# Kernel tuning notes

Hardware: AMD Instinct MI355X
Metric: run time of the kernel (lower is better)

## Reference

```python
import jax, jax.numpy as jnp
import numpy as np

N_NODES = 50000
N_EDGES = 200000
EMB = 256
N_LAYERS = 2
PRED_IN = 2 * EMB + 2 * N_LAYERS * EMB  # 1536


def _glorot(key, shape):
    fan_in, fan_out = shape
    lim = (6.0 / (fan_in + fan_out)) ** 0.5
    return jax.random.uniform(key, shape, jnp.float32, -lim, lim)


def setup_inputs() -> dict:
    key = jax.random.key(0)
    ks = jax.random.split(key, 16)
    inp = {
        "entity_embd": jax.random.normal(ks[0], (N_NODES, EMB), jnp.float32),
        "edge_attr": jax.random.normal(ks[1], (N_EDGES, EMB), jnp.float32),
        "q_embd": jax.random.normal(ks[2], (1, EMB), jnp.float32),
        "noise": jax.random.uniform(ks[3], (N_EDGES, 1), jnp.float32, 1e-10, 1.0 - 1e-10),
        # proj_reverse: Linear(emb,emb) -> ReLU -> Linear(emb,emb)
        "W_pr1": _glorot(ks[4], (EMB, EMB)), "b_pr1": jnp.zeros((EMB,), jnp.float32),
        "W_pr2": _glorot(ks[5], (EMB, EMB)), "b_pr2": jnp.zeros((EMB,), jnp.float32),
        # SAGE layers: Linear(concat[self, agg]) per layer
        "sage_W0": _glorot(ks[6], (2 * EMB, EMB)), "sage_b0": jnp.zeros((EMB,), jnp.float32),
        "sage_W1": _glorot(ks[7], (2 * EMB, EMB)), "sage_b1": jnp.zeros((EMB,), jnp.float32),
        # pred: Linear(pred_in, emb) -> ReLU -> Linear(emb, 1)
        "pred_W1": _glorot(ks[8], (PRED_IN, EMB)), "pred_b1": jnp.zeros((EMB,), jnp.float32),
        "pred_W2": _glorot(ks[9], (EMB, 1)), "pred_b2": jnp.zeros((1,), jnp.float32),
        "edge_index": jax.random.randint(ks[10], (2, N_EDGES), 0, N_NODES, jnp.int64),
    }
    return inp


def _segment_mean(msg, dst, num_nodes):
    s = jax.ops.segment_sum(msg, dst, num_segments=num_nodes)
    cnt = jax.ops.segment_sum(jnp.ones((dst.shape[0], 1), msg.dtype), dst, num_segments=num_nodes)
    return s / jnp.maximum(cnt, 1.0)


def reference(entity_embd, edge_attr, q_embd, noise,
              W_pr1, b_pr1, W_pr2, b_pr2,
              sage_W0, sage_b0, sage_W1, sage_b1,
              pred_W1, pred_b1, pred_W2, pred_b2,
              edge_index):
    h_id, t_id = edge_index[0], edge_index[1]
    # bidirectional edge list: original + reversed
    ei = jnp.concatenate([edge_index, edge_index[::-1]], axis=1)  # [2, 2E]
    src, dst = ei[0], ei[1]
    # reverse-edge feature projection
    ea_rev = jax.nn.relu(edge_attr @ W_pr1 + b_pr1) @ W_pr2 + b_pr2
    h_r = jnp.concatenate([edge_attr, ea_rev], axis=0)  # [2E, EMB]
    # SAGE backbone: mean-aggregate (src + edge feat), concat with self, linear+relu
    x = entity_embd
    outs = []
    for W, b in ((sage_W0, sage_b0), (sage_W1, sage_b1)):
        msg = x[src] + h_r                                # [2E, EMB]
        agg = _segment_mean(msg, dst, N_NODES)            # [N, EMB]
        x = jax.nn.relu(jnp.concatenate([x, agg], axis=1) @ W + b)
        outs.append(x)
    h_e = jnp.concatenate(outs, axis=1)  # [N, N_LAYERS*EMB]
    q = jnp.broadcast_to(q_embd, (N_EDGES, EMB))
    h_triple = jnp.concatenate([q, h_e[h_id], edge_attr, h_e[t_id]], axis=1)  # [E, 1536]
    logits = jax.nn.relu(h_triple @ pred_W1 + pred_b1) @ pred_W2 + pred_b2    # [E, 1]
    # idp-bern sampling (training=True, temp=1)
    rn = jnp.log(noise) - jnp.log(1.0 - noise)
    sampled = jax.nn.sigmoid(logits + rn)
    return (logits, sampled)
```

## Files before the change

### kernel.cpp

```cpp
#include <hip/hip_runtime.h>
#include <math.h>


namespace {
constexpr int E    = 200000;
constexpr int NV   = 50000;
constexpr int D    = 256;
constexpr int TWOE = 2 * E;
}

typedef __attribute__((ext_vector_type(8))) _Float16 f16x8;
typedef __attribute__((ext_vector_type(4))) _Float16 f16x4;
typedef __attribute__((ext_vector_type(16))) float f32x16;

#define MFMA16(a, b, c) __builtin_amdgcn_mfma_f32_32x32x16_f16((a), (b), (c), 0, 0, 0)

typedef const __attribute__((address_space(1))) void* gas_t;
typedef __attribute__((address_space(3))) void* las_t;

__device__ inline void gload16(const void* g, void* l) {
  __builtin_amdgcn_global_load_lds((gas_t)g, (las_t)l, 16, 0, 0);
}

__global__ void k_detect(const void* ei_raw, int* flag) {
  __shared__ int bad;
  if (threadIdx.x == 0) bad = 0;
  __syncthreads();
  const long long* p = (const long long*)ei_raw;
  long long v = p[threadIdx.x];
  if (v < 0 || v >= (long long)NV) atomicOr(&bad, 1);
  __syncthreads();
  if (threadIdx.x == 0) *flag = bad ? 0 : 1;
}

__global__ void k_convert(const void* ei_raw, const int* __restrict__ flag,
                          int* __restrict__ ei32) {
  int i = blockIdx.x * 256 + threadIdx.x;
  if (i >= TWOE) return;
  if (*flag) ei32[i] = (int)((const long long*)ei_raw)[i];
  else       ei32[i] = ((const int*)ei_raw)[i];
}

__global__ void k_deg(const int* __restrict__ ei32, int* __restrict__ deg) {
  int de = blockIdx.x * 256 + threadIdx.x;
  if (de >= TWOE) return;
  int dst = (de < E) ? ei32[E + de] : ei32[de - E];
  atomicAdd(&deg[dst], 1);
}

__global__ __launch_bounds__(1024) void k_scan(const int* __restrict__ deg,
                                               int* __restrict__ off) {
  __shared__ int wsum[16];
  __shared__ int carryS;
  int tid = threadIdx.x;
  int lane = tid & 63, wv = tid >> 6;
  if (tid == 0) carryS = 0;
  __syncthreads();
  for (int base = 0; base < NV; base += 1024) {
    int i = base + tid;
    int v = (i < NV) ? deg[i] : 0;
    int s = v;
#pragma unroll
    for (int d = 1; d < 64; d <<= 1) {
      int t = __shfl_up(s, d);
      if (lane >= d) s += t;
    }
    if (lane == 63) wsum[wv] = s;
    int carry = carryS;
    __syncthreads();
    if (wv == 0) {
      int ws = (lane < 16) ? wsum[lane] : 0;
#pragma unroll
      for (int d = 1; d < 16; d <<= 1) {
        int t = __shfl_up(ws, d);
        if (lane >= d) ws += t;
      }
      if (lane < 16) wsum[lane] = ws;
    }
    __syncthreads();
    int wexcl = (wv == 0) ? 0 : wsum[wv - 1];
    if (i < NV) off[i] = carry + wexcl + s - v;
    if (tid == 1023) carryS = carry + wsum[15];
    __syncthreads();
  }
  if (tid == 0) off[NV] = carryS;
}

__global__ void k_fill(const int* __restrict__ ei32, const int* __restrict__ off,
                       int* __restrict__ cursor, int* __restrict__ eidA,
                       int* __restrict__ srcA) {
  int de = blockIdx.x * 256 + threadIdx.x;
  if (de >= TWOE) return;
  int dst = (de < E) ? ei32[E + de] : ei32[de - E];
  int p = atomicAdd(&cursor[dst], 1);
  int idx = off[dst] + p;
  eidA[idx] = de;
  srcA[idx] = ei32[de];
}

__global__ void k_rinv(const int* __restrict__ off, float* __restrict__ rinv) {
  int n = blockIdx.x * 256 + threadIdx.x;
  if (n < NV) {
    int d = off[n + 1] - off[n];
    rinv[n] = 1.f / fmaxf((float)d, 1.f);
  }
}

__global__ void k_conv16(const float* __restrict__ x, _Float16* __restrict__ y,
                         int n8) {
  int i = blockIdx.x * 256 + threadIdx.x;
  if (i >= n8) return;
  const float4* p = (const float4*)x;
  float4 a = p[2 * i], b = p[2 * i + 1];
  f16x8 o;
  o[0] = (_Float16)a.x; o[1] = (_Float16)a.y; o[2] = (_Float16)a.z; o[3] = (_Float16)a.w;
  o[4] = (_Float16)b.x; o[5] = (_Float16)b.y; o[6] = (_Float16)b.z; o[7] = (_Float16)b.w;
  ((f16x8*)y)[i] = o;
}

__global__ __launch_bounds__(256) void k_gath_h(
    const _Float16* __restrict__ ea16, const _Float16* __restrict__ tmp16,
    const _Float16* __restrict__ ent16,
    const int* __restrict__ eidA, const int* __restrict__ srcA,
    const int* __restrict__ off,
    _Float16* __restrict__ hsum16, _Float16* __restrict__ hid16,
    _Float16* __restrict__ xsum16, float* __restrict__ degrev) {
  int n = blockIdx.x * 8 + (threadIdx.x >> 5);
  if (n >= NV) return;
  int l = threadIdx.x & 31;
  float fs[8], hv[8], xs[8];
#pragma unroll
  for (int k2 = 0; k2 < 8; k2++) { fs[k2] = 0.f; hv[k2] = 0.f; xs[k2] = 0.f; }
  int o0 = off[n], o1 = off[n + 1];
  int dr = 0;
#pragma unroll 2
  for (int j = o0; j < o1; j++) {
    int de = eidA[j];
    int src = srcA[j];
    f16x8 xv = ((const f16x8*)(ent16 + (size_t)src * D))[l];
#pragma unroll
    for (int k2 = 0; k2 < 8; k2++) xs[k2] += (float)xv[k2];
    if (de < E) {
      f16x8 v = ((const f16x8*)(ea16 + (size_t)de * D))[l];
#pragma unroll
      for (int k2 = 0; k2 < 8; k2++) fs[k2] += (float)v[k2];
    } else {
      f16x8 v = ((const f16x8*)(tmp16 + (size_t)(de - E) * D))[l];
#pragma unroll
      for (int k2 = 0; k2 < 8; k2++) hv[k2] += (float)v[k2];
      dr++;
    }
  }
  f16x8 of, oh, ox;
#pragma unroll
  for (int k2 = 0; k2 < 8; k2++) {
    of[k2] = (_Float16)fs[k2]; oh[k2] = (_Float16)hv[k2]; ox[k2] = (_Float16)xs[k2];
  }
  ((f16x8*)(hsum16 + (size_t)n * D))[l] = of;
  ((f16x8*)(hid16 + (size_t)n * D))[l] = oh;
  ((f16x8*)(xsum16 + (size_t)n * D))[l] = ox;
  if (l == 0) degrev[n] = (float)dr;
}

__global__ __launch_bounds__(256) void k_agg(
    const _Float16* __restrict__ x16, const int* __restrict__ srcA,
    const int* __restrict__ off, const _Float16* __restrict__ hsum16,
    const float* __restrict__ rinv, _Float16* __restrict__ agg16) {
  int n = blockIdx.x * 8 + (threadIdx.x >> 5);
  if (n >= NV) return;
  int l = threadIdx.x & 31;
  f16x8 h = ((const f16x8*)(hsum16 + (size_t)n * D))[l];
  float s[8];
#pragma unroll
  for (int k2 = 0; k2 < 8; k2++) s[k2] = (float)h[k2];
  int o0 = off[n], o1 = off[n + 1];
#pragma unroll 4
  for (int j = o0; j < o1; j++) {
    int src = srcA[j];
    f16x8 v = ((const f16x8*)(x16 + (size_t)src * D))[l];
#pragma unroll
    for (int k2 = 0; k2 < 8; k2++) s[k2] += (float)v[k2];
  }
  float r = rinv[n];
  f16x8 o;
#pragma unroll
  for (int k2 = 0; k2 < 8; k2++) o[k2] = (_Float16)(s[k2] * r);
  ((f16x8*)(agg16 + (size_t)n * D))[l] = o;
}

__global__ __launch_bounds__(256) void k_wprep(const float* __restrict__ W,
                                               _Float16* __restrict__ Wf) {
  __shared__ float tl[32][260];
  int tid = threadIdx.x;
  int k0 = blockIdx.x * 32;
#pragma unroll
  for (int i = 0; i < 32; i++) tl[i][tid] = W[(size_t)(k0 + i) * 256 + tid];
  __syncthreads();
  f16x8* WfV = (f16x8*)Wf;
#pragma unroll
  for (int kg = 0; kg < 4; kg++) {
    f16x8 p;
#pragma unroll
    for (int j = 0; j < 8; j++) p[j] = (_Float16)tl[kg * 8 + j][tid];
    WfV[(size_t)((k0 >> 3) + kg) * 256 + tid] = p;
  }
}

__global__ void k_qw(const float* __restrict__ q, const float* __restrict__ W1,
                     const float* __restrict__ b1, float* __restrict__ qW) {
  __shared__ float ql[D];
  int n = threadIdx.x;
  ql[n] = q[n];
  __syncthreads();
  float s = b1[n];
  for (int k = 0; k < D; k++) s += ql[k] * W1[(size_t)k * D + n];
  qW[n] = s;
}

enum AM { AF16, AF16D };
enum EP { EP_RELU16, EP_ADDC, EP_HE2, EP_PROJ2 };

template<int AMODE>
__device__ inline void stageA(const _Float16* __restrict__ A0,
                              const _Float16* __restrict__ A1,
                              int m0, int t, int tid, _Float16* ldsbuf) {
  const _Float16* src;
  int kbase;
  if (AMODE == AF16D && t >= 4) { src = A1; kbase = (t - 4) * 64; }
  else                          { src = A0; kbase = t * 64; }
  const int l  = tid & 63;
  const int w  = tid >> 6;
  const int r8 = l >> 3;
  const int kg = (l & 7) ^ r8;
#pragma unroll
  for (int j = 0; j < 2; j++) {
    const int c = w * 2 + j;
    const int row = c * 8 + r8;
    gload16(src + (size_t)(m0 + row) * 256 + kbase + kg * 8,
            ldsbuf + c * 512);
  }
}

template<int AMODE, int EPI>
__global__ __launch_bounds__(256, ((EPI == EP_HE2 || EPI == EP_PROJ2) ? 2 : 4))
void k_gemm(
    const _Float16* __restrict__ A0, const _Float16* __restrict__ A1,
    const _Float16* __restrict__ addm16, const _Float16* __restrict__ xs16,
    const float* __restrict__ degrev, const float* __restrict__ rinv,
    const _Float16* __restrict__ Wf, const _Float16* __restrict__ Wf2,
    const float* __restrict__ bias, const float* __restrict__ qW,
    _Float16* __restrict__ o16a, _Float16* __restrict__ o16b, int M, int K) {
  constexpr bool DUAL = (EPI == EP_HE2 || EPI == EP_PROJ2);
  __shared__ _Float16 AS[2 * 4096];
  const int tid = threadIdx.x;
  const int w = tid >> 6;
  const int lane31 = tid & 31;
  const int hw = (tid >> 5) & 1;
  const int m0 = blockIdx.x * 64;
  const int col0 = (w << 6) + lane31;
  const int col1 = col0 + 32;

  f32x16 acc[2][2], acc2[2][2];
#pragma unroll
  for (int a = 0; a < 2; a++)
#pragma unroll
    for (int b = 0; b < 2; b++)
#pragma unroll
      for (int i = 0; i < 16; i++) { acc[a][b][i] = 0.f; acc2[a][b][i] = 0.f; }

  const f16x8* WV  = (const f16x8*)Wf;
  const f16x8* WV2 = (const f16x8*)Wf2;
  const int nt = K >> 6;
  const int sw = lane31 & 7;

  stageA<AMODE>(A0, A1, m0, 0, tid, AS);
  __syncthreads();

  for (int t = 0; t < nt; ++t) {
    const int k0 = t * 64;
    f16x8 wb0[4], wb1[4], wc0[4], wc1[4];
#pragma unroll
    for (int ks = 0; ks < 4; ks++) {
      const int kgl = 2 * ks + hw;
      size_t wi = (size_t)((k0 >> 3) + kgl) * 256;
      wb0[ks] = WV[wi + col0];
      wb1[ks] = WV[wi + col1];
      if (DUAL) { wc0[ks] = WV2[wi + col0]; wc1[ks] = WV2[wi + col1]; }
    }
    __builtin_amdgcn_sched_barrier(0);
    if (t + 1 < nt)
      stageA<AMODE>(A0, A1, m0, t + 1, tid, AS + ((t + 1) & 1) * 4096);
    __builtin_amdgcn_sched_barrier(0);
    const f16x8* cb = (const f16x8*)(AS + (t & 1) * 4096);
#pragma unroll
    for (int ks = 0; ks < 4; ks++) {
      const int kgl = 2 * ks + hw;
      f16x8 a0 = cb[lane31 * 8 + (kgl ^ sw)];
      f16x8 a1 = cb[(lane31 + 32) * 8 + (kgl ^ sw)];
      acc[0][0] = MFMA16(a0, wb0[ks], acc[0][0]);
      acc[0][1] = MFMA16(a0, wb1[ks], acc[0][1]);
      acc[1][0] = MFMA16(a1, wb0[ks], acc[1][0]);
      acc[1][1] = MFMA16(a1, wb1[ks], acc[1][1]);
      if (DUAL) {
        acc2[0][0] = MFMA16(a0, wc0[ks], acc2[0][0]);
        acc2[0][1] = MFMA16(a0, wc1[ks], acc2[0][1]);
        acc2[1][0] = MFMA16(a1, wc0[ks], acc2[1][0]);
        acc2[1][1] = MFMA16(a1, wc1[ks], acc2[1][1]);
      }
    }
    __syncthreads();
  }

  if (EPI == EP_RELU16) {
    float b0v = bias[col0], b1v = bias[col1];
#pragma unroll
    for (int rf = 0; rf < 2; rf++)
#pragma unroll
      for (int g = 0; g < 4; g++)
#pragma unroll
        for (int qq = 0; qq < 4; qq++) {
          int row = m0 + 32 * rf + qq + 8 * g + 4 * hw;
          if (row < M) {
            o16a[(size_t)row * 256 + col0] =
                (_Float16)fmaxf(acc[rf][0][4 * g + qq] + b0v, 0.f);
            o16a[(size_t)row * 256 + col1] =
                (_Float16)fmaxf(acc[rf][1][4 * g + qq] + b1v, 0.f);
          }
        }
  }
  if (EPI == EP_ADDC) {
    float b0v = bias[col0], b1v = bias[col1];
#pragma unroll
    for (int rf = 0; rf < 2; rf++)
#pragma unroll
      for (int g = 0; g < 4; g++)
#pragma unroll
        for (int qq = 0; qq < 4; qq++) {
          int row = m0 + 32 * rf + qq + 8 * g + 4 * hw;
          if (row < M) {
            float dr = degrev[row], rv = rinv[row];
            size_t i0 = (size_t)row * 256 + col0;
            size_t i1 = (size_t)row * 256 + col1;
            float h0 = acc[rf][0][4 * g + qq] + (float)addm16[i0] + dr * b0v;
            float h1 = acc[rf][1][4 * g + qq] + (float)addm16[i1] + dr * b1v;
            o16a[i0] = (_Float16)h0;
            o16a[i1] = (_Float16)h1;
            o16b[i0] = (_Float16)((h0 + (float)xs16[i0]) * rv);
            o16b[i1] = (_Float16)((h1 + (float)xs16[i1]) * rv);
          }
        }
  }
  if (EPI == EP_HE2) {
#pragma unroll
    for (int rf = 0; rf < 2; rf++)
#pragma unroll
      for (int g = 0; g < 4; g++)
#pragma unroll
        for (int qq = 0; qq < 4; qq++) {
          int row = m0 + 32 * rf + qq + 8 * g + 4 * hw;
          if (row < M) {
            o16a[(size_t)row * 256 + col0] = (_Float16)acc[rf][0][4 * g + qq];
            o16a[(size_t)row * 256 + col1] = (_Float16)acc[rf][1][4 * g + qq];
            o16b[(size_t)row * 256 + col0] = (_Float16)acc2[rf][0][4 * g + qq];
            o16b[(size_t)row * 256 + col1] = (_Float16)acc2[rf][1][4 * g + qq];
          }
        }
  }
  if (EPI == EP_PROJ2) {
    float b0v = bias[col0], b1v = bias[col1];
    float q0 = qW[col0], q1 = qW[col1];
#pragma unroll
    for (int rf = 0; rf < 2; rf++)
#pragma unroll
      for (int g = 0; g < 4; g++)
#pragma unroll
        for (int qq = 0; qq < 4; qq++) {
          int row = m0 + 32 * rf + qq + 8 * g + 4 * hw;
          if (row < M) {
            o16a[(size_t)row * 256 + col0] =
                (_Float16)fmaxf(acc[rf][0][4 * g + qq] + b0v, 0.f);
            o16a[(size_t)row * 256 + col1] =
                (_Float16)fmaxf(acc[rf][1][4 * g + qq] + b1v, 0.f);
            o16b[(size_t)row * 256 + col0] = (_Float16)(acc2[rf][0][4 * g + qq] + q0);
            o16b[(size_t)row * 256 + col1] = (_Float16)(acc2[rf][1][4 * g + qq] + q1);
          }
        }
  }
}

__global__ __launch_bounds__(256) void k_edge(
    const _Float16* __restrict__ ea2q, const _Float16* __restrict__ HEh,
    const _Float16* __restrict__ HEt, const int* __restrict__ ei32,
    const float* __restrict__ pW2, const float* __restrict__ pb2,
    const float* __restrict__ noise, float* __restrict__ dout) {
  int e = blockIdx.x * 8 + (threadIdx.x >> 5);
  int l = threadIdx.x & 31;
  int h = ei32[e], t = ei32[E + e];
  f16x8 a  = ((const f16x8*)(ea2q + (size_t)e * 256))[l];
  f16x8 hv = ((const f16x8*)(HEh + (size_t)h * 256))[l];
  f16x8 tv = ((const f16x8*)(HEt + (size_t)t * 256))[l];
  const float4* wp = (const float4*)(pW2 + l * 8);
  float4 w0 = wp[0], w1 = wp[1];
  float wv[8] = {w0.x, w0.y, w0.z, w0.w, w1.x, w1.y, w1.z, w1.w};
  float s = 0.f;
#pragma unroll
  for (int j = 0; j < 8; j++)
    s += fmaxf((float)a[j] + (float)hv[j] + (float)tv[j], 0.f) * wv[j];
#pragma unroll
  for (int m = 1; m <= 16; m <<= 1) s += __shfl_xor(s, m);
  if (l == 0) {
    float lg = s + pb2[0];
    float nz = noise[e];
    float rn = logf(nz) - logf(1.f - nz);
    dout[e] = lg;
    dout[E + e] = 1.f / (1.f + expf(-(lg + rn)));
  }
}

extern "C" void kernel_launch(void* const* d_in, const int* in_sizes, int n_in,
                              void* d_out, int out_size, void* d_ws, size_t ws_size,
                              hipStream_t stream) {
  const float* entity = (const float*)d_in[0];
  const float* ea     = (const float*)d_in[1];
  const float* q      = (const float*)d_in[2];
  const float* noise  = (const float*)d_in[3];
  const float* W_pr1  = (const float*)d_in[4];
  const float* b_pr1  = (const float*)d_in[5];
  const float* W_pr2  = (const float*)d_in[6];
  const float* b_pr2  = (const float*)d_in[7];
  const float* sW0    = (const float*)d_in[8];
  const float* sb0    = (const float*)d_in[9];
  const float* sW1    = (const float*)d_in[10];
  const float* sb1    = (const float*)d_in[11];
  const float* pW1    = (const float*)d_in[12];
  const float* pb1    = (const float*)d_in[13];
  const float* pW2    = (const float*)d_in[14];
  const float* pb2    = (const float*)d_in[15];
  const void*  ei_raw = d_in[16];

  char* ws = (char*)d_ws;
  const size_t EDH = (size_t)E * D * 2;
  const size_t NDH = (size_t)NV * D * 2;
  const size_t PAD = 64 * 256 * 2;
  size_t off_b = 0;
  char* r0  = ws + off_b; off_b += EDH + PAD;
  char* r1a = ws + off_b; off_b += EDH + PAD;
  char* r1b = ws + off_b; off_b += EDH + PAD;
  char* r2  = ws + off_b; off_b += 2 * NDH + PAD;
  char* r3  = ws + off_b; off_b += NDH + PAD;
  char* r4  = ws + off_b; off_b += NDH + PAD;
  char* r5  = ws + off_b; off_b += NDH + PAD;
  char* r6  = ws + off_b; off_b += NDH + PAD;
  auto alloc_w = [&](int K) { _Float16* p = (_Float16*)(ws + off_b);
                              off_b += (size_t)K * 256 * 2; return p; };
  _Float16* Wpr1f = alloc_w(256);
  _Float16* Wpr2f = alloc_w(256);
  _Float16* sW0f  = alloc_w(512);
  _Float16* sW1f  = alloc_w(512);
  _Float16* Whehf = alloc_w(512);
  _Float16* Whetf = alloc_w(512);
  _Float16* Weaf  = alloc_w(256);
  float* rinv   = (float*)(ws + off_b); off_b += (size_t)NV * 4;
  float* degrev = (float*)(ws + off_b); off_b += (size_t)NV * 4;
  float* qW     = (float*)(ws + off_b); off_b += 1024;
  int*   ei32   = (int*)(ws + off_b);   off_b += (size_t)TWOE * 4;
  int*   eidA   = (int*)(ws + off_b);   off_b += (size_t)TWOE * 4;
  int*   srcA   = (int*)(ws + off_b);   off_b += (size_t)TWOE * 4;
  int*   offA   = (int*)(ws + off_b);   off_b += (size_t)(NV + 1) * 4;
  int*   deg    = (int*)(ws + off_b);   off_b += (size_t)NV * 4;
  int*   cursor = (int*)(ws + off_b);   off_b += (size_t)NV * 4;
  int*   flag   = (int*)(ws + off_b);   off_b += 64;

  _Float16* ea16   = (_Float16*)r0;
  _Float16* tmp16  = (_Float16*)r1a;
  _Float16* ea2q16 = (_Float16*)r1b;
  _Float16* hsum16 = (_Float16*)r2;
  _Float16* HEh16  = (_Float16*)r2;
  _Float16* HEt16  = (_Float16*)(r2 + NDH);
  _Float16* hid16  = (_Float16*)r3;
  _Float16* agg016 = (_Float16*)r3;
  _Float16* agg16  = (_Float16*)r3;
  _Float16* ent16  = (_Float16*)r4;
  _Float16* out116 = (_Float16*)r4;
  _Float16* out016 = (_Float16*)r5;
  _Float16* xsum16 = (_Float16*)r6;

  k_detect<<<1, 256, 0, stream>>>(ei_raw, flag);
  k_convert<<<(TWOE + 255) / 256, 256, 0, stream>>>(ei_raw, flag, ei32);
  hipMemsetAsync(deg, 0, (size_t)NV * 4, stream);
  hipMemsetAsync(cursor, 0, (size_t)NV * 4, stream);
  k_deg<<<(TWOE + 255) / 256, 256, 0, stream>>>(ei32, deg);
  k_scan<<<1, 1024, 0, stream>>>(deg, offA);
  k_fill<<<(TWOE + 255) / 256, 256, 0, stream>>>(ei32, offA, cursor, eidA, srcA);
  k_rinv<<<(NV + 255) / 256, 256, 0, stream>>>(offA, rinv);

  k_wprep<<<256 / 32, 256, 0, stream>>>(W_pr1, Wpr1f);
  k_wprep<<<256 / 32, 256, 0, stream>>>(W_pr2, Wpr2f);
  k_wprep<<<512 / 32, 256, 0, stream>>>(sW0, sW0f);
  k_wprep<<<512 / 32, 256, 0, stream>>>(sW1, sW1f);
  k_wprep<<<512 / 32, 256, 0, stream>>>(pW1 + 256 * 256, Whehf);
  k_wprep<<<512 / 32, 256, 0, stream>>>(pW1 + 1024 * 256, Whetf);
  k_wprep<<<256 / 32, 256, 0, stream>>>(pW1 + 768 * 256, Weaf);
  k_conv16<<<(NV * D / 8 + 255) / 256, 256, 0, stream>>>(entity, ent16, NV * D / 8);
  k_conv16<<<(E * D / 8 + 255) / 256, 256, 0, stream>>>(ea, ea16, E * D / 8);
  k_qw<<<1, 256, 0, stream>>>(q, pW1, pb1, qW);

  k_gemm<AF16, EP_PROJ2><<<E / 64, 256, 0, stream>>>(
      ea16, nullptr, nullptr, nullptr, nullptr, nullptr, Wpr1f, Weaf,
      b_pr1, qW, tmp16, ea2q16, E, 256);

  k_gath_h<<<(NV + 7) / 8, 256, 0, stream>>>(
      ea16, tmp16, ent16, eidA, srcA, offA, hsum16, hid16, xsum16, degrev);

  k_gemm<AF16, EP_ADDC><<<(NV + 63) / 64, 256, 0, stream>>>(
      hid16, nullptr, hsum16, xsum16, degrev, rinv, Wpr2f, nullptr,
      b_pr2, nullptr, hsum16, agg016, NV, 256);

  k_gemm<AF16D, EP_RELU16><<<(NV + 63) / 64, 256, 0, stream>>>(
      ent16, agg016, nullptr, nullptr, nullptr, nullptr, sW0f, nullptr,
      sb0, nullptr, out016, nullptr, NV, 512);
  k_agg<<<(NV + 7) / 8, 256, 0, stream>>>(out016, srcA, offA, hsum16, rinv, agg16);
  k_gemm<AF16D, EP_RELU16><<<(NV + 63) / 64, 256, 0, stream>>>(
      out016, agg16, nullptr, nullptr, nullptr, nullptr, sW1f, nullptr,
      sb1, nullptr, out116, nullptr, NV, 512);

  k_gemm<AF16D, EP_HE2><<<(NV + 63) / 64, 256, 0, stream>>>(
      out016, out116, nullptr, nullptr, nullptr, nullptr, Whehf, Whetf,
      nullptr, nullptr, HEh16, HEt16, NV, 512);

  k_edge<<<E / 8, 256, 0, stream>>>(ea2q16, HEh16, HEt16, ei32, pW2, pb2, noise,
                                    (float*)d_out);
}
```

Before: 632.7 us.

## Fuse chained node-level GEMMs into two kernels keeping intermediates in LDS

```diff
diff --git a/kernel.cpp b/kernel.cpp
--- a/kernel.cpp
+++ b/kernel.cpp
@@ -218,7 +218,6 @@
 }
 
 enum AM { AF16, AF16D };
-enum EP { EP_RELU16, EP_ADDC, EP_HE2, EP_PROJ2 };
 
 template<int AMODE>
 __device__ inline void stageA(const _Float16* __restrict__ A0,
@@ -241,16 +240,11 @@
   }
 }
 
-template<int AMODE, int EPI>
-__global__ __launch_bounds__(256, ((EPI == EP_HE2 || EPI == EP_PROJ2) ? 2 : 4))
-void k_gemm(
-    const _Float16* __restrict__ A0, const _Float16* __restrict__ A1,
-    const _Float16* __restrict__ addm16, const _Float16* __restrict__ xs16,
-    const float* __restrict__ degrev, const float* __restrict__ rinv,
+__global__ __launch_bounds__(256, 2) void k_proj2(
+    const _Float16* __restrict__ A0,
     const _Float16* __restrict__ Wf, const _Float16* __restrict__ Wf2,
     const float* __restrict__ bias, const float* __restrict__ qW,
-    _Float16* __restrict__ o16a, _Float16* __restrict__ o16b, int M, int K) {
-  constexpr bool DUAL = (EPI == EP_HE2 || EPI == EP_PROJ2);
+    _Float16* __restrict__ o16a, _Float16* __restrict__ o16b, int M) {
   __shared__ _Float16 AS[2 * 4096];
   const int tid = threadIdx.x;
   const int w = tid >> 6;
@@ -259,6 +253,7 @@
   const int m0 = blockIdx.x * 64;
   const int col0 = (w << 6) + lane31;
   const int col1 = col0 + 32;
+  const int sw = lane31 & 7;
 
   f32x16 acc[2][2], acc2[2][2];
 #pragma unroll
@@ -270,26 +265,21 @@
 
   const f16x8* WV  = (const f16x8*)Wf;
   const f16x8* WV2 = (const f16x8*)Wf2;
-  const int nt = K >> 6;
-  const int sw = lane31 & 7;
-
-  stageA<AMODE>(A0, A1, m0, 0, tid, AS);
+
+  stageA<AF16>(A0, nullptr, m0, 0, tid, AS);
   __syncthreads();
-
-  for (int t = 0; t < nt; ++t) {
+  for (int t = 0; t < 4; ++t) {
     const int k0 = t * 64;
     f16x8 wb0[4], wb1[4], wc0[4], wc1[4];
 #pragma unroll
     for (int ks = 0; ks < 4; ks++) {
       const int kgl = 2 * ks + hw;
       size_t wi = (size_t)((k0 >> 3) + kgl) * 256;
-      wb0[ks] = WV[wi + col0];
-      wb1[ks] = WV[wi + col1];
-      if (DUAL) { wc0[ks] = WV2[wi + col0]; wc1[ks] = WV2[wi + col1]; }
+      wb0[ks] = WV[wi + col0];  wb1[ks] = WV[wi + col1];
+      wc0[ks] = WV2[wi + col0]; wc1[ks] = WV2[wi + col1];
     }
     __builtin_amdgcn_sched_barrier(0);
-    if (t + 1 < nt)
-      stageA<AMODE>(A0, A1, m0, t + 1, tid, AS + ((t + 1) & 1) * 4096);
+    if (t + 1 < 4) stageA<AF16>(A0, nullptr, m0, t + 1, tid, AS + ((t + 1) & 1) * 4096);
     __builtin_amdgcn_sched_barrier(0);
     const f16x8* cb = (const f16x8*)(AS + (t & 1) * 4096);
 #pragma unroll
@@ -301,18 +291,275 @@
       acc[0][1] = MFMA16(a0, wb1[ks], acc[0][1]);
       acc[1][0] = MFMA16(a1, wb0[ks], acc[1][0]);
       acc[1][1] = MFMA16(a1, wb1[ks], acc[1][1]);
-      if (DUAL) {
+      acc2[0][0] = MFMA16(a0, wc0[ks], acc2[0][0]);
+      acc2[0][1] = MFMA16(a0, wc1[ks], acc2[0][1]);
+      acc2[1][0] = MFMA16(a1, wc0[ks], acc2[1][0]);
+      acc2[1][1] = MFMA16(a1, wc1[ks], acc2[1][1]);
+    }
+    __syncthreads();
+  }
+  float b0v = bias[col0], b1v = bias[col1];
+  float q0 = qW[col0], q1 = qW[col1];
+#pragma unroll
+  for (int rf = 0; rf < 2; rf++)
+#pragma unroll
+    for (int g = 0; g < 4; g++)
+#pragma unroll
+      for (int qq = 0; qq < 4; qq++) {
+        int row = m0 + 32 * rf + qq + 8 * g + 4 * hw;
+        if (row < M) {
+          o16a[(size_t)row * 256 + col0] =
+              (_Float16)fmaxf(acc[rf][0][4 * g + qq] + b0v, 0.f);
+          o16a[(size_t)row * 256 + col1] =
+              (_Float16)fmaxf(acc[rf][1][4 * g + qq] + b1v, 0.f);
+          o16b[(size_t)row * 256 + col0] = (_Float16)(acc2[rf][0][4 * g + qq] + q0);
+          o16b[(size_t)row * 256 + col1] = (_Float16)(acc2[rf][1][4 * g + qq] + q1);
+        }
+      }
+}
+
+__global__ __launch_bounds__(256, 2) void k_fuse0(
+    const _Float16* __restrict__ hid16, const _Float16* __restrict__ ent16,
+    _Float16* __restrict__ hsum16, const _Float16* __restrict__ xsum16,
+    const float* __restrict__ degrev, const float* __restrict__ rinv,
+    const _Float16* __restrict__ Wpr2f, const float* __restrict__ bpr2,
+    const _Float16* __restrict__ sW0f, const float* __restrict__ sb0,
+    _Float16* __restrict__ out016, int M) {
+  __shared__ _Float16 AS[2 * 4096];
+  __shared__ _Float16 AGG[4 * 4096];
+  const int tid = threadIdx.x;
+  const int w = tid >> 6;
+  const int lane31 = tid & 31;
+  const int hw = (tid >> 5) & 1;
+  const int m0 = blockIdx.x * 64;
+  const int col0 = (w << 6) + lane31;
+  const int col1 = col0 + 32;
+  const int sw = lane31 & 7;
+  const int kgA = lane31 >> 3, kjA = lane31 & 7;
+
+  f32x16 acc[2][2];
+#pragma unroll
+  for (int a = 0; a < 2; a++)
+#pragma unroll
+    for (int b = 0; b < 2; b++)
+#pragma unroll
+      for (int i = 0; i < 16; i++) acc[a][b][i] = 0.f;
+
+  {
+    const f16x8* WV = (const f16x8*)Wpr2f;
+    stageA<AF16>(hid16, nullptr, m0, 0, tid, AS);
+    __syncthreads();
+    for (int t = 0; t < 4; ++t) {
+      const int k0 = t * 64;
+      f16x8 wb0[4], wb1[4];
+#pragma unroll
+      for (int ks = 0; ks < 4; ks++) {
+        const int kgl = 2 * ks + hw;
+        size_t wi = (size_t)((k0 >> 3) + kgl) * 256;
+        wb0[ks] = WV[wi + col0]; wb1[ks] = WV[wi + col1];
+      }
+      __builtin_amdgcn_sched_barrier(0);
+      if (t + 1 < 4) stageA<AF16>(hid16, nullptr, m0, t + 1, tid, AS + ((t + 1) & 1) * 4096);
+      __builtin_amdgcn_sched_barrier(0);
+      const f16x8* cb = (const f16x8*)(AS + (t & 1) * 4096);
+#pragma unroll
+      for (int ks = 0; ks < 4; ks++) {
+        const int kgl = 2 * ks + hw;
+        f16x8 a0 = cb[lane31 * 8 + (kgl ^ sw)];
+        f16x8 a1 = cb[(lane31 + 32) * 8 + (kgl ^ sw)];
+        acc[0][0] = MFMA16(a0, wb0[ks], acc[0][0]);
+        acc[0][1] = MFMA16(a0, wb1[ks], acc[0][1]);
+        acc[1][0] = MFMA16(a1, wb0[ks], acc[1][0]);
+        acc[1][1] = MFMA16(a1, wb1[ks], acc[1][1]);
+      }
+      __syncthreads();
+    }
+  }
+  stageA<AF16>(ent16, nullptr, m0, 0, tid, AS);
+  {
+    float b0v = bpr2[col0], b1v = bpr2[col1];
+    _Float16* AGGw = AGG + (w << 12);
+#pragma unroll
+    for (int rf = 0; rf < 2; rf++)
+#pragma unroll
+      for (int g = 0; g < 4; g++)
+#pragma unroll
+        for (int qq = 0; qq < 4; qq++) {
+          int rowloc = 32 * rf + qq + 8 * g + 4 * hw;
+          int row = m0 + rowloc;
+          float a0 = 0.f, a1 = 0.f;
+          if (row < M) {
+            float dr = degrev[row], rv = rinv[row];
+            size_t i0 = (size_t)row * 256 + col0;
+            size_t i1 = (size_t)row * 256 + col1;
+            float h0 = acc[rf][0][4 * g + qq] + (float)hsum16[i0] + dr * b0v;
+            float h1 = acc[rf][1][4 * g + qq] + (float)hsum16[i1] + dr * b1v;
+            hsum16[i0] = (_Float16)h0;
+            hsum16[i1] = (_Float16)h1;
+            a0 = (h0 + (float)xsum16[i0]) * rv;
+            a1 = (h1 + (float)xsum16[i1]) * rv;
+          }
+          int rsw = rowloc & 7;
+          AGGw[rowloc * 64 + ((kgA ^ rsw) << 3) + kjA] = (_Float16)a0;
+          AGGw[rowloc * 64 + (((kgA + 4) ^ rsw) << 3) + kjA] = (_Float16)a1;
+          acc[rf][0][4 * g + qq] = 0.f;
+          acc[rf][1][4 * g + qq] = 0.f;
+        }
+  }
+  __syncthreads();
+  {
+    const f16x8* WV = (const f16x8*)sW0f;
+    for (int tt = 0; tt < 8; ++tt) {
+      f16x8 wb0[4], wb1[4];
+#pragma unroll
+      for (int ks = 0; ks < 4; ks++) {
+        const int kgl = 2 * ks + hw;
+        size_t wi = (size_t)(tt * 8 + kgl) * 256;
+        wb0[ks] = WV[wi + col0]; wb1[ks] = WV[wi + col1];
+      }
+      __builtin_amdgcn_sched_barrier(0);
+      if (tt + 1 < 4) stageA<AF16>(ent16, nullptr, m0, tt + 1, tid, AS + ((tt + 1) & 1) * 4096);
+      __builtin_amdgcn_sched_barrier(0);
+      const f16x8* cb = (tt < 4) ? (const f16x8*)(AS + (tt & 1) * 4096)
+                                 : (const f16x8*)(AGG + ((tt - 4) << 12));
+#pragma unroll
+      for (int ks = 0; ks < 4; ks++) {
+        const int kgl = 2 * ks + hw;
+        f16x8 a0 = cb[lane31 * 8 + (kgl ^ sw)];
+        f16x8 a1 = cb[(lane31 + 32) * 8 + (kgl ^ sw)];
+        acc[0][0] = MFMA16(a0, wb0[ks], acc[0][0]);
+        acc[0][1] = MFMA16(a0, wb1[ks], acc[0][1]);
+        acc[1][0] = MFMA16(a1, wb0[ks], acc[1][0]);
+        acc[1][1] = MFMA16(a1, wb1[ks], acc[1][1]);
+      }
+      __syncthreads();
+    }
+    float b0v = sb0[col0], b1v = sb0[col1];
+#pragma unroll
+    for (int rf = 0; rf < 2; rf++)
+#pragma unroll
+      for (int g = 0; g < 4; g++)
+#pragma unroll
+        for (int qq = 0; qq < 4; qq++) {
+          int row = m0 + 32 * rf + qq + 8 * g + 4 * hw;
+          if (row < M) {
+            out016[(size_t)row * 256 + col0] =
+                (_Float16)fmaxf(acc[rf][0][4 * g + qq] + b0v, 0.f);
+            out016[(size_t)row * 256 + col1] =
+                (_Float16)fmaxf(acc[rf][1][4 * g + qq] + b1v, 0.f);
+          }
+        }
+  }
+}
+
+__global__ __launch_bounds__(256, 2) void k_fuse1(
+    const _Float16* __restrict__ out016, const _Float16* __restrict__ agg16,
+    const _Float16* __restrict__ sW1f, const float* __restrict__ sb1,
+    const _Float16* __restrict__ Whehf, const _Float16* __restrict__ Whetf,
+    _Float16* __restrict__ HEh16, _Float16* __restrict__ HEt16, int M) {
+  __shared__ _Float16 AS[2 * 4096];
+  __shared__ _Float16 OUT[4 * 4096];
+  const int tid = threadIdx.x;
+  const int w = tid >> 6;
+  const int lane31 = tid & 31;
+  const int hw = (tid >> 5) & 1;
+  const int m0 = blockIdx.x * 64;
+  const int col0 = (w << 6) + lane31;
+  const int col1 = col0 + 32;
+  const int sw = lane31 & 7;
+  const int kgA = lane31 >> 3, kjA = lane31 & 7;
+
+  f32x16 acc[2][2], acc2[2][2];
+#pragma unroll
+  for (int a = 0; a < 2; a++)
+#pragma unroll
+    for (int b = 0; b < 2; b++)
+#pragma unroll
+      for (int i = 0; i < 16; i++) { acc[a][b][i] = 0.f; acc2[a][b][i] = 0.f; }
+
+  {
+    const f16x8* WV = (const f16x8*)sW1f;
+    stageA<AF16D>(out016, agg16, m0, 0, tid, AS);
+    __syncthreads();
+    for (int t = 0; t < 8; ++t) {
+      f16x8 wb0[4], wb1[4];
+#pragma unroll
+      for (int ks = 0; ks < 4; ks++) {
+        const int kgl = 2 * ks + hw;
+        size_t wi = (size_t)(t * 8 + kgl) * 256;
+        wb0[ks] = WV[wi + col0]; wb1[ks] = WV[wi + col1];
+      }
+      __builtin_amdgcn_sched_barrier(0);
+      if (t + 1 < 8) stageA<AF16D>(out016, agg16, m0, t + 1, tid, AS + ((t + 1) & 1) * 4096);
+      __builtin_amdgcn_sched_barrier(0);
+      const f16x8* cb = (const f16x8*)(AS + (t & 1) * 4096);
+#pragma unroll
+      for (int ks = 0; ks < 4; ks++) {
+        const int kgl = 2 * ks + hw;
+        f16x8 a0 = cb[lane31 * 8 + (kgl ^ sw)];
+        f16x8 a1 = cb[(lane31 + 32) * 8 + (kgl ^ sw)];
+        acc[0][0] = MFMA16(a0, wb0[ks], acc[0][0]);
+        acc[0][1] = MFMA16(a0, wb1[ks], acc[0][1]);
+        acc[1][0] = MFMA16(a1, wb0[ks], acc[1][0]);
+        acc[1][1] = MFMA16(a1, wb1[ks], acc[1][1]);
+      }
+      __syncthreads();
+    }
+  }
+  stageA<AF16>(out016, nullptr, m0, 0, tid, AS);
+  {
+    float b0v = sb1[col0], b1v = sb1[col1];
+    _Float16* OUTw = OUT + (w << 12);
+#pragma unroll
+    for (int rf = 0; rf < 2; rf++)
+#pragma unroll
+      for (int g = 0; g < 4; g++)
+#pragma unroll
+        for (int qq = 0; qq < 4; qq++) {
+          int rowloc = 32 * rf + qq + 8 * g + 4 * hw;
+          float v0 = fmaxf(acc[rf][0][4 * g + qq] + b0v, 0.f);
+          float v1 = fmaxf(acc[rf][1][4 * g + qq] + b1v, 0.f);
+          int rsw = rowloc & 7;
+          OUTw[rowloc * 64 + ((kgA ^ rsw) << 3) + kjA] = (_Float16)v0;
+          OUTw[rowloc * 64 + (((kgA + 4) ^ rsw) << 3) + kjA] = (_Float16)v1;
+          acc[rf][0][4 * g + qq] = 0.f;
+          acc[rf][1][4 * g + qq] = 0.f;
+        }
+  }
+  __syncthreads();
+  {
+    const f16x8* WV  = (const f16x8*)Whehf;
+    const f16x8* WV2 = (const f16x8*)Whetf;
+    for (int tt = 0; tt < 8; ++tt) {
+      f16x8 wb0[4], wb1[4], wc0[4], wc1[4];
+#pragma unroll
+      for (int ks = 0; ks < 4; ks++) {
+        const int kgl = 2 * ks + hw;
+        size_t wi = (size_t)(tt * 8 + kgl) * 256;
+        wb0[ks] = WV[wi + col0];  wb1[ks] = WV[wi + col1];
+        wc0[ks] = WV2[wi + col0]; wc1[ks] = WV2[wi + col1];
+      }
+      __builtin_amdgcn_sched_barrier(0);
+      if (tt + 1 < 4) stageA<AF16>(out016, nullptr, m0, tt + 1, tid, AS + ((tt + 1) & 1) * 4096);
+      __builtin_amdgcn_sched_barrier(0);
+      const f16x8* cb = (tt < 4) ? (const f16x8*)(AS + (tt & 1) * 4096)
+                                 : (const f16x8*)(OUT + ((tt - 4) << 12));
+#pragma unroll
+      for (int ks = 0; ks < 4; ks++) {
+        const int kgl = 2 * ks + hw;
+        f16x8 a0 = cb[lane31 * 8 + (kgl ^ sw)];
+        f16x8 a1 = cb[(lane31 + 32) * 8 + (kgl ^ sw)];
+        acc[0][0] = MFMA16(a0, wb0[ks], acc[0][0]);
+        acc[0][1] = MFMA16(a0, wb1[ks], acc[0][1]);
+        acc[1][0] = MFMA16(a1, wb0[ks], acc[1][0]);
+        acc[1][1] = MFMA16(a1, wb1[ks], acc[1][1]);
         acc2[0][0] = MFMA16(a0, wc0[ks], acc2[0][0]);
         acc2[0][1] = MFMA16(a0, wc1[ks], acc2[0][1]);
         acc2[1][0] = MFMA16(a1, wc0[ks], acc2[1][0]);
         acc2[1][1] = MFMA16(a1, wc1[ks], acc2[1][1]);
       }
-    }
-    __syncthreads();
-  }
-
-  if (EPI == EP_RELU16) {
-    float b0v = bias[col0], b1v = bias[col1];
+      __syncthreads();
+    }
 #pragma unroll
     for (int rf = 0; rf < 2; rf++)
 #pragma unroll
@@ -321,68 +568,10 @@
         for (int qq = 0; qq < 4; qq++) {
           int row = m0 + 32 * rf + qq + 8 * g + 4 * hw;
           if (row < M) {
-            o16a[(size_t)row * 256 + col0] =
-                (_Float16)fmaxf(acc[rf][0][4 * g + qq] + b0v, 0.f);
-            o16a[(size_t)row * 256 + col1] =
-                (_Float16)fmaxf(acc[rf][1][4 * g + qq] + b1v, 0.f);
-          }
-        }
-  }
-  if (EPI == EP_ADDC) {
-    float b0v = bias[col0], b1v = bias[col1];
-#pragma unroll
-    for (int rf = 0; rf < 2; rf++)
-#pragma unroll
-      for (int g = 0; g < 4; g++)
-#pragma unroll
-        for (int qq = 0; qq < 4; qq++) {
-          int row = m0 + 32 * rf + qq + 8 * g + 4 * hw;
-          if (row < M) {
-            float dr = degrev[row], rv = rinv[row];
-            size_t i0 = (size_t)row * 256 + col0;
-            size_t i1 = (size_t)row * 256 + col1;
-            float h0 = acc[rf][0][4 * g + qq] + (float)addm16[i0] + dr * b0v;
-            float h1 = acc[rf][1][4 * g + qq] + (float)addm16[i1] + dr * b1v;
-            o16a[i0] = (_Float16)h0;
-            o16a[i1] = (_Float16)h1;
-            o16b[i0] = (_Float16)((h0 + (float)xs16[i0]) * rv);
-            o16b[i1] = (_Float16)((h1 + (float)xs16[i1]) * rv);
-          }
-        }
-  }
-  if (EPI == EP_HE2) {
-#pragma unroll
-    for (int rf = 0; rf < 2; rf++)
-#pragma unroll
-      for (int g = 0; g < 4; g++)
-#pragma unroll
-        for (int qq = 0; qq < 4; qq++) {
-          int row = m0 + 32 * rf + qq + 8 * g + 4 * hw;
-          if (row < M) {
-            o16a[(size_t)row * 256 + col0] = (_Float16)acc[rf][0][4 * g + qq];
-            o16a[(size_t)row * 256 + col1] = (_Float16)acc[rf][1][4 * g + qq];
-            o16b[(size_t)row * 256 + col0] = (_Float16)acc2[rf][0][4 * g + qq];
-            o16b[(size_t)row * 256 + col1] = (_Float16)acc2[rf][1][4 * g + qq];
-          }
-        }
-  }
-  if (EPI == EP_PROJ2) {
-    float b0v = bias[col0], b1v = bias[col1];
-    float q0 = qW[col0], q1 = qW[col1];
-#pragma unroll
-    for (int rf = 0; rf < 2; rf++)
-#pragma unroll
-      for (int g = 0; g < 4; g++)
-#pragma unroll
-        for (int qq = 0; qq < 4; qq++) {
-          int row = m0 + 32 * rf + qq + 8 * g + 4 * hw;
-          if (row < M) {
-            o16a[(size_t)row * 256 + col0] =
-                (_Float16)fmaxf(acc[rf][0][4 * g + qq] + b0v, 0.f);
-            o16a[(size_t)row * 256 + col1] =
-                (_Float16)fmaxf(acc[rf][1][4 * g + qq] + b1v, 0.f);
-            o16b[(size_t)row * 256 + col0] = (_Float16)(acc2[rf][0][4 * g + qq] + q0);
-            o16b[(size_t)row * 256 + col1] = (_Float16)(acc2[rf][1][4 * g + qq] + q1);
+            HEh16[(size_t)row * 256 + col0] = (_Float16)acc[rf][0][4 * g + qq];
+            HEh16[(size_t)row * 256 + col1] = (_Float16)acc[rf][1][4 * g + qq];
+            HEt16[(size_t)row * 256 + col0] = (_Float16)acc2[rf][0][4 * g + qq];
+            HEt16[(size_t)row * 256 + col1] = (_Float16)acc2[rf][1][4 * g + qq];
           }
         }
   }
@@ -478,10 +667,8 @@
   _Float16* HEh16  = (_Float16*)r2;
   _Float16* HEt16  = (_Float16*)(r2 + NDH);
   _Float16* hid16  = (_Float16*)r3;
-  _Float16* agg016 = (_Float16*)r3;
   _Float16* agg16  = (_Float16*)r3;
   _Float16* ent16  = (_Float16*)r4;
-  _Float16* out116 = (_Float16*)r4;
   _Float16* out016 = (_Float16*)r5;
   _Float16* xsum16 = (_Float16*)r6;
 
@@ -505,28 +692,20 @@
   k_conv16<<<(E * D / 8 + 255) / 256, 256, 0, stream>>>(ea, ea16, E * D / 8);
   k_qw<<<1, 256, 0, stream>>>(q, pW1, pb1, qW);
 
-  k_gemm<AF16, EP_PROJ2><<<E / 64, 256, 0, stream>>>(
-      ea16, nullptr, nullptr, nullptr, nullptr, nullptr, Wpr1f, Weaf,
-      b_pr1, qW, tmp16, ea2q16, E, 256);
+  k_proj2<<<E / 64, 256, 0, stream>>>(ea16, Wpr1f, Weaf, b_pr1, qW,
+                                      tmp16, ea2q16, E);
 
   k_gath_h<<<(NV + 7) / 8, 256, 0, stream>>>(
       ea16, tmp16, ent16, eidA, srcA, offA, hsum16, hid16, xsum16, degrev);
 
-  k_gemm<AF16, EP_ADDC><<<(NV + 63) / 64, 256, 0, stream>>>(
-      hid16, nullptr, hsum16, xsum16, degrev, rinv, Wpr2f, nullptr,
-      b_pr2, nullptr, hsum16, agg016, NV, 256);
-
-  k_gemm<AF16D, EP_RELU16><<<(NV + 63) / 64, 256, 0, stream>>>(
-      ent16, agg016, nullptr, nullptr, nullptr, nullptr, sW0f, nullptr,
-      sb0, nullptr, out016, nullptr, NV, 512);
+  k_fuse0<<<(NV + 63) / 64, 256, 0, stream>>>(
+      hid16, ent16, hsum16, xsum16, degrev, rinv, Wpr2f, b_pr2,
+      sW0f, sb0, out016, NV);
+
   k_agg<<<(NV + 7) / 8, 256, 0, stream>>>(out016, srcA, offA, hsum16, rinv, agg16);
-  k_gemm<AF16D, EP_RELU16><<<(NV + 63) / 64, 256, 0, stream>>>(
-      out016, agg16, nullptr, nullptr, nullptr, nullptr, sW1f, nullptr,
-      sb1, nullptr, out116, nullptr, NV, 512);
-
-  k_gemm<AF16D, EP_HE2><<<(NV + 63) / 64, 256, 0, stream>>>(
-      out016, out116, nullptr, nullptr, nullptr, nullptr, Whehf, Whetf,
-      nullptr, nullptr, HEh16, HEt16, NV, 512);
+
+  k_fuse1<<<(NV + 63) / 64, 256, 0, stream>>>(
+      out016, agg16, sW1f, sb1, Whehf, Whetf, HEh16, HEt16, NV);
 
   k_edge<<<E / 8, 256, 0, stream>>>(ea2q16, HEh16, HEt16, ei32, pW2, pb2, noise,
                                     (float*)d_out);
```

Result: no change. 625.8 us (-1.1%).
